# Kernel optimization log

Hardware: AMD Instinct MI355X
Metric: run time of the kernel (lower is better)

## Reference

```python
import jax, jax.numpy as jnp
import numpy as np

B, V, D = 4096, 20, 768


def _conv1d_k3(x, w, b):
    # x: [B, V, D]; single-channel conv1d, kernel=3, padding=1 (torch cross-correlation)
    xp = jnp.pad(x, ((0, 0), (0, 0), (1, 1)))
    return w[0] * xp[..., :-2] + w[1] * xp[..., 1:-1] + w[2] * xp[..., 2:] + b[0]


def setup_inputs() -> dict:
    key = jax.random.key(0)
    ks = jax.random.split(key, 10)
    s = 0.02  # small init scale for weights
    return {
        "text_features": jax.random.normal(ks[0], (B, D), jnp.float32),
        "viewport_features": jax.random.normal(ks[1], (B, V, D), jnp.float32),
        "W1": jax.random.normal(ks[2], (D, D), jnp.float32) * s,
        "b1": jax.random.normal(ks[3], (D,), jnp.float32) * s,
        "W2": jax.random.normal(ks[4], (D, D), jnp.float32) * s,
        "b2": jax.random.normal(ks[5], (D,), jnp.float32) * s,
        "cw1": jax.random.normal(ks[6], (3,), jnp.float32) * 0.5,
        "cb1": jax.random.normal(ks[7], (1,), jnp.float32) * 0.1,
        "cw2": jax.random.normal(ks[8], (3,), jnp.float32) * 0.5,
        "cb2": jax.random.normal(ks[9], (1,), jnp.float32) * 0.1,
    }


def reference(text_features, viewport_features, W1, b1, W2, b2, cw1, cb1, cw2, cb2):
    # Batched over all 20 viewports at once (original loops over i).
    fli_norm = jax.nn.softmax(viewport_features, axis=-1)          # [B,V,D]
    # torch Linear: x @ W.T + b
    m1 = jnp.einsum('bvd,ed->bve', fli_norm, W1) + b1              # mlp1(fli_norm)
    m2 = jnp.einsum('bvd,ed->bve', fli_norm, W2) + b2              # mlp2(fli_norm)
    fused = jax.nn.relu(text_features[:, None, :] * m1 + m2)       # [B,V,D]
    fused = _conv1d_k3(fused, cw1, cb1)
    fused = jax.nn.relu(fused)
    fused = _conv1d_k3(fused, cw2, cb2)
    return fused.reshape(B, V * D)                                 # torch.cat along dim=1
```

## Files before the change

### kernel.cpp

```cpp
#include <hip/hip_runtime.h>

typedef unsigned short u16;
typedef __attribute__((ext_vector_type(8))) short short8;
typedef __attribute__((ext_vector_type(4))) float f32x4;

#define Bn 4096
#define Vn 20
#define Dn 768
#define Mn (Bn * Vn)
#define Nn (2 * Dn)

#define BM 256
#define BNt 256
#define NTILES (Nn / BNt)
#define GRID ((Mn / BM) * NTILES)

typedef __attribute__((address_space(1))) void GV;
typedef __attribute__((address_space(3))) void LV;

__device__ __forceinline__ u16 f2bf(float f) {
  union { float f; unsigned u; } v; v.f = f;
  unsigned r = v.u + 0x7FFFu + ((v.u >> 16) & 1u);
  return (u16)(r >> 16);
}
__device__ __forceinline__ float bf2f(u16 x) {
  union { unsigned u; float f; } v; v.u = ((unsigned)x) << 16; return v.f;
}

__device__ __forceinline__ int lds_off(int r, int hi) {
  return (r >> 1) * 64 + (r & 1) * 32 + ((hi ^ ((r >> 1) & 3)) * 8);
}

__global__ __launch_bounds__(192) void softmax_k(const float* __restrict__ vf,
                                                 u16* __restrict__ X) {
  size_t row = blockIdx.x;
  const float4* p = (const float4*)(vf + row * Dn);
  int t = threadIdx.x;
  float4 v = p[t];
  float mx = fmaxf(fmaxf(v.x, v.y), fmaxf(v.z, v.w));
  #pragma unroll
  for (int off = 32; off; off >>= 1) mx = fmaxf(mx, __shfl_xor(mx, off));
  __shared__ float rr[3];
  __shared__ float rs[3];
  int wv = t >> 6, ln = t & 63;
  if (!ln) rr[wv] = mx;
  __syncthreads();
  mx = fmaxf(fmaxf(rr[0], rr[1]), rr[2]);
  float e0 = __expf(v.x - mx), e1 = __expf(v.y - mx);
  float e2 = __expf(v.z - mx), e3 = __expf(v.w - mx);
  float s = e0 + e1 + e2 + e3;
  #pragma unroll
  for (int off = 32; off; off >>= 1) s += __shfl_xor(s, off);
  if (!ln) rs[wv] = s;
  __syncthreads();
  float inv = 1.0f / (rs[0] + rs[1] + rs[2]);
  ushort4 o;
  o.x = f2bf(e0 * inv); o.y = f2bf(e1 * inv);
  o.z = f2bf(e2 * inv); o.w = f2bf(e3 * inv);
  ((ushort4*)(X + row * Dn))[t] = o;
}

__global__ __launch_bounds__(256) void build_wt_k(const float* __restrict__ W1,
                                                  const float* __restrict__ W2,
                                                  u16* __restrict__ Wt) {
  int idx = blockIdx.x * 256 + threadIdx.x;
  if (idx >= Dn * Dn) return;
  int j = idx / Dn, d = idx - j * Dn;
  int b = j >> 5, c = j & 31;
  Wt[(size_t)(b * 64 + c) * Dn + d]      = f2bf(W1[(size_t)j * Dn + d]);
  Wt[(size_t)(b * 64 + 32 + c) * Dn + d] = f2bf(W2[(size_t)j * Dn + d]);
}

__global__ __launch_bounds__(512, 2) void gemm_fuse_k(
    const u16* __restrict__ X, const u16* __restrict__ Wt,
    const float* __restrict__ b1, const float* __restrict__ b2,
    const float* __restrict__ text, float* __restrict__ out,
    u16* __restrict__ seam,
    const float* __restrict__ cw1, const float* __restrict__ cb1,
    const float* __restrict__ cw2, const float* __restrict__ cb2) {
  __shared__ __align__(16) u16 smem[65536];

  const int h = blockIdx.x;
  const int lin = (h & 7) * (GRID / 8) + (h >> 3);
  const int by = lin / NTILES, bx = lin - by * NTILES;
  const int brow = by * BM;

  const int t = threadIdx.x, w = t >> 6, l = t & 63;
  const int lo = l & 15, hi = l >> 4;
  const int wrr = w >> 2, wcc = w & 3;

  int offA[8], offB[4];
  #pragma unroll
  for (int m = 0; m < 8; ++m) offA[m] = lds_off(wrr * 128 + m * 16 + lo, hi);
  #pragma unroll
  for (int n = 0; n < 4; ++n) offB[n] = lds_off(wcc * 64 + n * 16 + lo, hi);

  const u16* gA[2];
  const u16* gB[2];
  #pragma unroll
  for (int ii = 0; ii < 2; ++ii) {
    int q = ii * 512 + t;
    int rp = q >> 3, half = (q >> 2) & 1, kc = (q & 3) ^ (rp & 3);
    gA[ii] = X + (size_t)(brow + rp * 2 + half) * Dn + kc * 8;
    gB[ii] = Wt + (size_t)(bx * BNt + rp * 2 + half) * Dn + kc * 8;
  }

#define STG_A(DST, KOFF) do { _Pragma("unroll")                                \
    for (int ii = 0; ii < 2; ++ii)                                             \
      __builtin_amdgcn_global_load_lds((GV*)(gA[ii] + (KOFF)),                 \
          (LV*)(smem + (DST) + (ii * 512 + w * 64) * 8), 16, 0, 0); } while (0)
#define STG_B(DST, KOFF) do { _Pragma("unroll")                                \
    for (int ii = 0; ii < 2; ++ii)                                             \
      __builtin_amdgcn_global_load_lds((GV*)(gB[ii] + (KOFF)),                 \
          (LV*)(smem + (DST) + (ii * 512 + w * 64) * 8), 16, 0, 0); } while (0)

  STG_A(0, 0);              STG_B(16384, 0);
  STG_A(32768, 64);         STG_B(49152, 64);
  STG_A(8192, 32);          STG_B(24576, 32);
  STG_A(40960, 96);         STG_B(57344, 96);
  asm volatile("s_waitcnt vmcnt(12)" ::: "memory");
  __builtin_amdgcn_s_barrier();

  f32x4 acc[8][4] = {};
  short8 af[8], bb0, bb1;

#define PH(SB, KH, NH, NEWA, STG, VM) do {                                     \
    if (NEWA) { _Pragma("unroll") for (int m = 0; m < 8; ++m)                  \
      af[m] = *(const short8*)(smem + (SB) + (KH) * 8192 + offA[m]); }         \
    bb0 = *(const short8*)(smem + (SB) + 16384 + (KH) * 8192 + offB[(NH)*2]);  \
    bb1 = *(const short8*)(smem + (SB) + 16384 + (KH) * 8192 + offB[(NH)*2+1]);\
    STG;                                                                       \
    __builtin_amdgcn_s_barrier();                                              \
    asm volatile("s_waitcnt lgkmcnt(0)" ::: "memory");                         \
    __builtin_amdgcn_sched_barrier(0);                                         \
    __builtin_amdgcn_s_setprio(1);                                             \
    _Pragma("unroll") for (int m = 0; m < 8; ++m) {                            \
      acc[m][(NH)*2]   = __builtin_amdgcn_mfma_f32_16x16x32_bf16(af[m], bb0, acc[m][(NH)*2],   0, 0, 0); \
      acc[m][(NH)*2+1] = __builtin_amdgcn_mfma_f32_16x16x32_bf16(af[m], bb1, acc[m][(NH)*2+1], 0, 0, 0); \
    }                                                                          \
    __builtin_amdgcn_s_setprio(0);                                             \
    VM;                                                                        \
    __builtin_amdgcn_s_barrier();                                              \
  } while (0)

#define VM4 asm volatile("s_waitcnt vmcnt(4)" ::: "memory")
#define VM0 asm volatile("s_waitcnt vmcnt(0)" ::: "memory")

  #pragma unroll
  for (int i = 0; i < 6; ++i) {
    const int ka = (2 * i + 1) * 64;
    const int kb = (2 * i + 2) * 64;
    PH(0, 0, 0, true,  if (i >= 1) STG_A(32768, ka),      ;  );
    PH(0, 0, 1, false, if (i >= 1) STG_B(49152, ka),      VM4);
    PH(0, 1, 0, true,  if (i >= 1) STG_A(40960, ka + 32), ;  );
    PH(0, 1, 1, false, if (i >= 1) STG_B(57344, ka + 32), VM4);
    PH(32768, 0, 0, true,  if (i <= 4) STG_A(0, kb),          ;  );
    PH(32768, 0, 1, false, if (i <= 4) STG_B(16384, kb),      if (i == 5) { VM0; } else { VM4; });
    PH(32768, 1, 0, true,  if (i <= 4) STG_A(8192, kb + 32),  ;  );
    PH(32768, 1, 1, false, if (i <= 4) STG_B(24576, kb + 32), if (i <= 4) { VM4; });
  }
#undef PH
#undef VM4
#undef VM0
#undef STG_A
#undef STG_B

  const float w10 = cw1[0], w11 = cw1[1], w12 = cw1[2], c1b = cb1[0];
  const float w20 = cw2[0], w21 = cw2[1], w22 = cw2[2], c2b = cb2[0];

  u16* fsm = smem;
  u16* tsm = smem + 32768;

  #pragma unroll
  for (int n = 0; n < 2; ++n) {
    const int cl = wcc * 32 + n * 16 + lo;
    const int e  = bx * 128 + cl;
    const float B1 = b1[e], B2 = b2[e];
    #pragma unroll
    for (int m = 0; m < 8; ++m) {
      const int rl = wrr * 128 + m * 16 + hi * 4;
      uint2 pk;
      u16* pku = (u16*)&pk;
      #pragma unroll
      for (int r = 0; r < 4; ++r) {
        const int gr = brow + rl + r;
        const float v1 = acc[m][n][r] + B1;
        const float v2 = acc[m][n + 2][r] + B2;
        const float tf = text[(size_t)(gr / Vn) * Dn + e];
        pku[r] = f2bf(fmaxf(tf * v1 + v2, 0.0f));
      }
      *(uint2*)(fsm + cl * 256 + (rl ^ ((cl & 31) << 3))) = pk;
      const int sidx = (cl < 4) ? cl : ((cl >= 124) ? cl - 120 : -1);
      if (sidx >= 0)
        *(uint2*)(seam + ((size_t)(by * 6 + bx) * 8 + sidx) * 256 + rl) = pk;
    }
  }
  __syncthreads();

  const int cl = t & 127, rb = t >> 7;
  const int cL = cl ? cl - 1 : 0, cR = (cl < 127) ? cl + 1 : 127;
  short8 tC[8];
  #pragma unroll
  for (int j = 0; j < 8; ++j) {
    const int R = rb * 64 + j * 8;
    short8 sL = *(const short8*)(fsm + cL * 256 + (R ^ ((cL & 31) << 3)));
    short8 sC = *(const short8*)(fsm + cl * 256 + (R ^ ((cl & 31) << 3)));
    short8 sR = *(const short8*)(fsm + cR * 256 + (R ^ ((cR & 31) << 3)));
    short8 o;
    #pragma unroll
    for (int k = 0; k < 8; ++k) {
      float a = bf2f((u16)sL[k]), b = bf2f((u16)sC[k]), c = bf2f((u16)sR[k]);
      float v = fmaxf(fmaf(w10, a, fmaf(w11, b, fmaf(w12, c, c1b))), 0.0f);
      o[k] = (short)f2bf(v);
    }
    *(short8*)(tsm + cl * 256 + (R ^ ((cl & 31) << 3))) = o;
    tC[j] = o;
  }
  __syncthreads();

  const bool wr_ok = (cl >= 2 && cl <= 125);
  #pragma unroll
  for (int j = 0; j < 8; ++j) {
    const int R = rb * 64 + j * 8;
    short8 tL = *(const short8*)(tsm + cL * 256 + (R ^ ((cL & 31) << 3)));
    short8 tR = *(const short8*)(tsm + cR * 256 + (R ^ ((cR & 31) << 3)));
    #pragma unroll
    for (int k = 0; k < 8; ++k) {
      float v = fmaf(w20, bf2f((u16)tL[k]),
                fmaf(w21, bf2f((u16)tC[j][k]),
                fmaf(w22, bf2f((u16)tR[k]), c2b)));
      if (wr_ok)
        out[(size_t)(brow + R + k) * Dn + bx * 128 + cl] = v;
    }
  }
}

__global__ __launch_bounds__(256) void seam_k(const u16* __restrict__ seam,
                                              float* __restrict__ out,
                                              const float* __restrict__ cw1,
                                              const float* __restrict__ cb1,
                                              const float* __restrict__ cw2,
                                              const float* __restrict__ cb2) {
  const int bid = blockIdx.x;
  const int by = bid / 6, bx = bid - by * 6;
  const int r = threadIdx.x;
  const float w10 = cw1[0], w11 = cw1[1], w12 = cw1[2], c1b = cb1[0];
  const float w20 = cw2[0], w21 = cw2[1], w22 = cw2[2], c2b = cb2[0];
  #define SM(B, I) bf2f(seam[((size_t)(B) * 8 + (I)) * 256 + r])
  float fm2 = 0.f, fm1 = 0.f, fR0 = 0.f, fR1 = 0.f;
  if (bx > 0) { fm2 = SM(bid - 1, 6); fm1 = SM(bid - 1, 7); }
  if (bx < 5) { fR0 = SM(bid + 1, 0); fR1 = SM(bid + 1, 1); }
  const float f0 = SM(bid, 0), f1 = SM(bid, 1), f2 = SM(bid, 2), f3 = SM(bid, 3);
  const float f124 = SM(bid, 4), f125 = SM(bid, 5), f126 = SM(bid, 6), f127 = SM(bid, 7);
  #undef SM
  #define C1(a, b, c) fmaxf(fmaf(w10, (a), fmaf(w11, (b), fmaf(w12, (c), c1b))), 0.0f)
  const float tm1  = (bx > 0) ? C1(fm2, fm1, f0) : 0.0f;
  const float t0   = C1(fm1, f0, f1);
  const float t1   = C1(f0, f1, f2);
  const float t2   = C1(f1, f2, f3);
  const float t125 = C1(f124, f125, f126);
  const float t126 = C1(f125, f126, f127);
  const float t127 = C1(f126, f127, fR0);
  const float t128 = (bx < 5) ? C1(f127, fR0, fR1) : 0.0f;
  #undef C1
  const size_t go = (size_t)(by * 256 + r) * Dn + bx * 128;
  out[go + 0]   = fmaf(w20, tm1,  fmaf(w21, t0,   fmaf(w22, t1,   c2b)));
  out[go + 1]   = fmaf(w20, t0,   fmaf(w21, t1,   fmaf(w22, t2,   c2b)));
  out[go + 126] = fmaf(w20, t125, fmaf(w21, t126, fmaf(w22, t127, c2b)));
  out[go + 127] = fmaf(w20, t126, fmaf(w21, t127, fmaf(w22, t128, c2b)));
}

extern "C" void kernel_launch(void* const* d_in, const int* in_sizes, int n_in,
                              void* d_out, int out_size, void* d_ws, size_t ws_size,
                              hipStream_t stream) {
  const float* text = (const float*)d_in[0];
  const float* vf   = (const float*)d_in[1];
  const float* W1   = (const float*)d_in[2];
  const float* b1   = (const float*)d_in[3];
  const float* W2   = (const float*)d_in[4];
  const float* b2   = (const float*)d_in[5];
  const float* cw1  = (const float*)d_in[6];
  const float* cb1  = (const float*)d_in[7];
  const float* cw2  = (const float*)d_in[8];
  const float* cb2  = (const float*)d_in[9];
  float* out = (float*)d_out;

  u16* X    = (u16*)d_ws;
  u16* Wt   = X + (size_t)Mn * Dn;
  u16* seam = Wt + (size_t)Nn * Dn;

  softmax_k<<<Mn, 192, 0, stream>>>(vf, X);
  build_wt_k<<<(Dn * Dn + 255) / 256, 256, 0, stream>>>(W1, W2, Wt);
  gemm_fuse_k<<<GRID, 512, 0, stream>>>(X, Wt, b1, b2, text, out, seam,
                                        cw1, cb1, cw2, cb2);
  seam_k<<<GRID, 256, 0, stream>>>(seam, out, cw1, cb1, cw2, cb2);
}
```

Measured before the change: 373.8 us.

## Shrink GEMM tile to 256x128 with simpler double-buffered K loop for occupancy

Halves the N tile of the fused GEMM (128 interleaved W1/W2 columns, 64 output features) and cuts LDS to 64KB so four blocks per CU can fit. The hand-scheduled 8-phase K pipeline is replaced by a simple two-slot double buffer over K chunks of 32. The conv epilogue, seam handling and seam kernel are rescaled to 64-column output tiles. In exchange each A tile is reloaded twice as often, more seam columns need fixup, and there is less MFMA work per barrier.

```diff
diff --git a/kernel.cpp b/kernel.cpp
--- a/kernel.cpp
+++ b/kernel.cpp
@@ -11,9 +11,12 @@
 #define Nn (2 * Dn)
 
 #define BM 256
-#define BNt 256
+#define BNt 128
+#define HK 32
+#define NHK (Dn / HK)
 #define NTILES (Nn / BNt)
 #define GRID ((Mn / BM) * NTILES)
+#define SLOTU 12288
 
 typedef __attribute__((address_space(1))) void GV;
 typedef __attribute__((address_space(3))) void LV;
@@ -29,6 +32,9 @@
 
 __device__ __forceinline__ int lds_off(int r, int hi) {
   return (r >> 1) * 64 + (r & 1) * 32 + ((hi ^ ((r >> 1) & 3)) * 8);
+}
+__device__ __forceinline__ int fsw(int c, int r) {
+  return c * 256 + (r ^ ((c & 31) << 3));
 }
 
 __global__ __launch_bounds__(192) void softmax_k(const float* __restrict__ vf,
@@ -71,14 +77,14 @@
   Wt[(size_t)(b * 64 + 32 + c) * Dn + d] = f2bf(W2[(size_t)j * Dn + d]);
 }
 
-__global__ __launch_bounds__(512, 2) void gemm_fuse_k(
+__global__ __launch_bounds__(512, 4) void gemm_fuse_k(
     const u16* __restrict__ X, const u16* __restrict__ Wt,
     const float* __restrict__ b1, const float* __restrict__ b2,
     const float* __restrict__ text, float* __restrict__ out,
     u16* __restrict__ seam,
     const float* __restrict__ cw1, const float* __restrict__ cb1,
     const float* __restrict__ cw2, const float* __restrict__ cb2) {
-  __shared__ __align__(16) u16 smem[65536];
+  __shared__ __align__(16) u16 smem[32768];
 
   const int h = blockIdx.x;
   const int lin = (h & 7) * (GRID / 8) + (h >> 3);
@@ -87,98 +93,80 @@
 
   const int t = threadIdx.x, w = t >> 6, l = t & 63;
   const int lo = l & 15, hi = l >> 4;
-  const int wrr = w >> 2, wcc = w & 3;
-
-  int offA[8], offB[4];
-  #pragma unroll
-  for (int m = 0; m < 8; ++m) offA[m] = lds_off(wrr * 128 + m * 16 + lo, hi);
-  #pragma unroll
-  for (int n = 0; n < 4; ++n) offB[n] = lds_off(wcc * 64 + n * 16 + lo, hi);
+  const int wrr = w >> 1, wcc = w & 1;
+
+  int offA[4], offB[4];
+  #pragma unroll
+  for (int m = 0; m < 4; ++m) offA[m] = lds_off(wrr * 64 + m * 16 + lo, hi);
+  #pragma unroll
+  for (int n = 0; n < 4; ++n) offB[n] = 8192 + lds_off(wcc * 64 + n * 16 + lo, hi);
 
   const u16* gA[2];
-  const u16* gB[2];
+  const u16* gB;
   #pragma unroll
   for (int ii = 0; ii < 2; ++ii) {
     int q = ii * 512 + t;
     int rp = q >> 3, half = (q >> 2) & 1, kc = (q & 3) ^ (rp & 3);
     gA[ii] = X + (size_t)(brow + rp * 2 + half) * Dn + kc * 8;
-    gB[ii] = Wt + (size_t)(bx * BNt + rp * 2 + half) * Dn + kc * 8;
-  }
-
-#define STG_A(DST, KOFF) do { _Pragma("unroll")                                \
+  }
+  {
+    int rp = t >> 3, half = (t >> 2) & 1, kc = (t & 3) ^ (rp & 3);
+    gB = Wt + (size_t)(bx * BNt + rp * 2 + half) * Dn + kc * 8;
+  }
+
+#define STAGE(SLOT, KOFF) do {                                                 \
+    _Pragma("unroll")                                                          \
     for (int ii = 0; ii < 2; ++ii)                                             \
       __builtin_amdgcn_global_load_lds((GV*)(gA[ii] + (KOFF)),                 \
-          (LV*)(smem + (DST) + (ii * 512 + w * 64) * 8), 16, 0, 0); } while (0)
-#define STG_B(DST, KOFF) do { _Pragma("unroll")                                \
-    for (int ii = 0; ii < 2; ++ii)                                             \
-      __builtin_amdgcn_global_load_lds((GV*)(gB[ii] + (KOFF)),                 \
-          (LV*)(smem + (DST) + (ii * 512 + w * 64) * 8), 16, 0, 0); } while (0)
-
-  STG_A(0, 0);              STG_B(16384, 0);
-  STG_A(32768, 64);         STG_B(49152, 64);
-  STG_A(8192, 32);          STG_B(24576, 32);
-  STG_A(40960, 96);         STG_B(57344, 96);
-  asm volatile("s_waitcnt vmcnt(12)" ::: "memory");
-  __builtin_amdgcn_s_barrier();
-
-  f32x4 acc[8][4] = {};
-  short8 af[8], bb0, bb1;
-
-#define PH(SB, KH, NH, NEWA, STG, VM) do {                                     \
-    if (NEWA) { _Pragma("unroll") for (int m = 0; m < 8; ++m)                  \
-      af[m] = *(const short8*)(smem + (SB) + (KH) * 8192 + offA[m]); }         \
-    bb0 = *(const short8*)(smem + (SB) + 16384 + (KH) * 8192 + offB[(NH)*2]);  \
-    bb1 = *(const short8*)(smem + (SB) + 16384 + (KH) * 8192 + offB[(NH)*2+1]);\
-    STG;                                                                       \
-    __builtin_amdgcn_s_barrier();                                              \
-    asm volatile("s_waitcnt lgkmcnt(0)" ::: "memory");                         \
-    __builtin_amdgcn_sched_barrier(0);                                         \
-    __builtin_amdgcn_s_setprio(1);                                             \
-    _Pragma("unroll") for (int m = 0; m < 8; ++m) {                            \
-      acc[m][(NH)*2]   = __builtin_amdgcn_mfma_f32_16x16x32_bf16(af[m], bb0, acc[m][(NH)*2],   0, 0, 0); \
-      acc[m][(NH)*2+1] = __builtin_amdgcn_mfma_f32_16x16x32_bf16(af[m], bb1, acc[m][(NH)*2+1], 0, 0, 0); \
-    }                                                                          \
-    __builtin_amdgcn_s_setprio(0);                                             \
-    VM;                                                                        \
-    __builtin_amdgcn_s_barrier();                                              \
+          (LV*)(smem + (SLOT) * SLOTU + (ii * 512 + t) * 8), 16, 0, 0);        \
+    __builtin_amdgcn_global_load_lds((GV*)(gB + (KOFF)),                       \
+        (LV*)(smem + (SLOT) * SLOTU + 8192 + t * 8), 16, 0, 0);                \
   } while (0)
 
-#define VM4 asm volatile("s_waitcnt vmcnt(4)" ::: "memory")
-#define VM0 asm volatile("s_waitcnt vmcnt(0)" ::: "memory")
-
-  #pragma unroll
-  for (int i = 0; i < 6; ++i) {
-    const int ka = (2 * i + 1) * 64;
-    const int kb = (2 * i + 2) * 64;
-    PH(0, 0, 0, true,  if (i >= 1) STG_A(32768, ka),      ;  );
-    PH(0, 0, 1, false, if (i >= 1) STG_B(49152, ka),      VM4);
-    PH(0, 1, 0, true,  if (i >= 1) STG_A(40960, ka + 32), ;  );
-    PH(0, 1, 1, false, if (i >= 1) STG_B(57344, ka + 32), VM4);
-    PH(32768, 0, 0, true,  if (i <= 4) STG_A(0, kb),          ;  );
-    PH(32768, 0, 1, false, if (i <= 4) STG_B(16384, kb),      if (i == 5) { VM0; } else { VM4; });
-    PH(32768, 1, 0, true,  if (i <= 4) STG_A(8192, kb + 32),  ;  );
-    PH(32768, 1, 1, false, if (i <= 4) STG_B(24576, kb + 32), if (i <= 4) { VM4; });
-  }
-#undef PH
-#undef VM4
-#undef VM0
-#undef STG_A
-#undef STG_B
+  STAGE(0, 0);
+  STAGE(1, HK);
+
+  f32x4 acc[4][4] = {};
+  short8 af[4], bfr[4];
+
+  #pragma unroll 2
+  for (int hk = 0; hk < NHK; ++hk) {
+    if (hk < NHK - 2) asm volatile("s_waitcnt vmcnt(3)" ::: "memory");
+    else              asm volatile("s_waitcnt vmcnt(0)" ::: "memory");
+    __builtin_amdgcn_s_barrier();
+    const u16* sa = smem + (hk & 1) * SLOTU;
+    #pragma unroll
+    for (int m = 0; m < 4; ++m) af[m]  = *(const short8*)(sa + offA[m]);
+    #pragma unroll
+    for (int n = 0; n < 4; ++n) bfr[n] = *(const short8*)(sa + offB[n]);
+    asm volatile("s_waitcnt lgkmcnt(0)" ::: "memory");
+    __builtin_amdgcn_sched_barrier(0);
+    __builtin_amdgcn_s_setprio(1);
+    #pragma unroll
+    for (int m = 0; m < 4; ++m)
+      #pragma unroll
+      for (int n = 0; n < 4; ++n)
+        acc[m][n] = __builtin_amdgcn_mfma_f32_16x16x32_bf16(af[m], bfr[n], acc[m][n], 0, 0, 0);
+    __builtin_amdgcn_s_setprio(0);
+    __builtin_amdgcn_s_barrier();
+    if (hk < NHK - 2) STAGE(hk & 1, (hk + 2) * HK);
+  }
+#undef STAGE
 
   const float w10 = cw1[0], w11 = cw1[1], w12 = cw1[2], c1b = cb1[0];
   const float w20 = cw2[0], w21 = cw2[1], w22 = cw2[2], c2b = cb2[0];
 
   u16* fsm = smem;
-  u16* tsm = smem + 32768;
+  u16* tsm = smem + 16384;
 
   #pragma unroll
   for (int n = 0; n < 2; ++n) {
     const int cl = wcc * 32 + n * 16 + lo;
-    const int e  = bx * 128 + cl;
+    const int e  = bx * 64 + cl;
     const float B1 = b1[e], B2 = b2[e];
     #pragma unroll
-    for (int m = 0; m < 8; ++m) {
-      const int rl = wrr * 128 + m * 16 + hi * 4;
+    for (int m = 0; m < 4; ++m) {
+      const int rl = wrr * 64 + m * 16 + hi * 4;
       uint2 pk;
       u16* pku = (u16*)&pk;
       #pragma unroll
@@ -189,48 +177,47 @@
         const float tf = text[(size_t)(gr / Vn) * Dn + e];
         pku[r] = f2bf(fmaxf(tf * v1 + v2, 0.0f));
       }
-      *(uint2*)(fsm + cl * 256 + (rl ^ ((cl & 31) << 3))) = pk;
-      const int sidx = (cl < 4) ? cl : ((cl >= 124) ? cl - 120 : -1);
+      *(uint2*)(fsm + fsw(cl, rl)) = pk;
+      const int sidx = (cl < 4) ? cl : ((cl >= 60) ? cl - 56 : -1);
       if (sidx >= 0)
-        *(uint2*)(seam + ((size_t)(by * 6 + bx) * 8 + sidx) * 256 + rl) = pk;
+        *(uint2*)(seam + ((size_t)(by * NTILES + bx) * 8 + sidx) * 256 + rl) = pk;
     }
   }
   __syncthreads();
 
-  const int cl = t & 127, rb = t >> 7;
-  const int cL = cl ? cl - 1 : 0, cR = (cl < 127) ? cl + 1 : 127;
-  short8 tC[8];
-  #pragma unroll
-  for (int j = 0; j < 8; ++j) {
-    const int R = rb * 64 + j * 8;
-    short8 sL = *(const short8*)(fsm + cL * 256 + (R ^ ((cL & 31) << 3)));
-    short8 sC = *(const short8*)(fsm + cl * 256 + (R ^ ((cl & 31) << 3)));
-    short8 sR = *(const short8*)(fsm + cR * 256 + (R ^ ((cR & 31) << 3)));
+  const int cl = t & 63, rb = t >> 6;
+  const int cL = cl ? cl - 1 : 0, cR = (cl < 63) ? cl + 1 : 63;
+  short8 tC[4];
+  #pragma unroll
+  for (int j = 0; j < 4; ++j) {
+    const int R = rb * 32 + j * 8;
+    short8 sL = *(const short8*)(fsm + fsw(cL, R));
+    short8 sC = *(const short8*)(fsm + fsw(cl, R));
+    short8 sR = *(const short8*)(fsm + fsw(cR, R));
     short8 o;
     #pragma unroll
     for (int k = 0; k < 8; ++k) {
       float a = bf2f((u16)sL[k]), b = bf2f((u16)sC[k]), c = bf2f((u16)sR[k]);
-      float v = fmaxf(fmaf(w10, a, fmaf(w11, b, fmaf(w12, c, c1b))), 0.0f);
-      o[k] = (short)f2bf(v);
+      o[k] = (short)f2bf(fmaxf(fmaf(w10, a, fmaf(w11, b, fmaf(w12, c, c1b))), 0.0f));
     }
-    *(short8*)(tsm + cl * 256 + (R ^ ((cl & 31) << 3))) = o;
+    *(short8*)(tsm + fsw(cl, R)) = o;
     tC[j] = o;
   }
   __syncthreads();
 
-  const bool wr_ok = (cl >= 2 && cl <= 125);
-  #pragma unroll
-  for (int j = 0; j < 8; ++j) {
-    const int R = rb * 64 + j * 8;
-    short8 tL = *(const short8*)(tsm + cL * 256 + (R ^ ((cL & 31) << 3)));
-    short8 tR = *(const short8*)(tsm + cR * 256 + (R ^ ((cR & 31) << 3)));
+  const bool wr_ok = (cl >= 2 && cl <= 61);
+  #pragma unroll
+  for (int j = 0; j < 4; ++j) {
+    const int R = rb * 32 + j * 8;
+    short8 tL = *(const short8*)(tsm + fsw(cL, R));
+    short8 tR = *(const short8*)(tsm + fsw(cR, R));
     #pragma unroll
     for (int k = 0; k < 8; ++k) {
       float v = fmaf(w20, bf2f((u16)tL[k]),
                 fmaf(w21, bf2f((u16)tC[j][k]),
                 fmaf(w22, bf2f((u16)tR[k]), c2b)));
       if (wr_ok)
-        out[(size_t)(brow + R + k) * Dn + bx * 128 + cl] = v;
+        out[(size_t)(brow + R + k) * Dn + bx * 64 + cl] = v;
     }
   }
 }
@@ -242,32 +229,32 @@
                                               const float* __restrict__ cw2,
                                               const float* __restrict__ cb2) {
   const int bid = blockIdx.x;
-  const int by = bid / 6, bx = bid - by * 6;
+  const int by = bid / NTILES, bx = bid - by * NTILES;
   const int r = threadIdx.x;
   const float w10 = cw1[0], w11 = cw1[1], w12 = cw1[2], c1b = cb1[0];
   const float w20 = cw2[0], w21 = cw2[1], w22 = cw2[2], c2b = cb2[0];
   #define SM(B, I) bf2f(seam[((size_t)(B) * 8 + (I)) * 256 + r])
   float fm2 = 0.f, fm1 = 0.f, fR0 = 0.f, fR1 = 0.f;
-  if (bx > 0) { fm2 = SM(bid - 1, 6); fm1 = SM(bid - 1, 7); }
-  if (bx < 5) { fR0 = SM(bid + 1, 0); fR1 = SM(bid + 1, 1); }
+  if (bx > 0)          { fm2 = SM(bid - 1, 6); fm1 = SM(bid - 1, 7); }
+  if (bx < NTILES - 1) { fR0 = SM(bid + 1, 0); fR1 = SM(bid + 1, 1); }
   const float f0 = SM(bid, 0), f1 = SM(bid, 1), f2 = SM(bid, 2), f3 = SM(bid, 3);
-  const float f124 = SM(bid, 4), f125 = SM(bid, 5), f126 = SM(bid, 6), f127 = SM(bid, 7);
+  const float f60 = SM(bid, 4), f61 = SM(bid, 5), f62 = SM(bid, 6), f63 = SM(bid, 7);
   #undef SM
   #define C1(a, b, c) fmaxf(fmaf(w10, (a), fmaf(w11, (b), fmaf(w12, (c), c1b))), 0.0f)
-  const float tm1  = (bx > 0) ? C1(fm2, fm1, f0) : 0.0f;
-  const float t0   = C1(fm1, f0, f1);
-  const float t1   = C1(f0, f1, f2);
-  const float t2   = C1(f1, f2, f3);
-  const float t125 = C1(f124, f125, f126);
-  const float t126 = C1(f125, f126, f127);
-  const float t127 = C1(f126, f127, fR0);
-  const float t128 = (bx < 5) ? C1(f127, fR0, fR1) : 0.0f;
+  const float tm1 = (bx > 0) ? C1(fm2, fm1, f0) : 0.0f;
+  const float t0  = C1(fm1, f0, f1);
+  const float t1  = C1(f0, f1, f2);
+  const float t2  = C1(f1, f2, f3);
+  const float t61 = C1(f60, f61, f62);
+  const float t62 = C1(f61, f62, f63);
+  const float t63 = C1(f62, f63, fR0);
+  const float t64 = (bx < NTILES - 1) ? C1(f63, fR0, fR1) : 0.0f;
   #undef C1
-  const size_t go = (size_t)(by * 256 + r) * Dn + bx * 128;
-  out[go + 0]   = fmaf(w20, tm1,  fmaf(w21, t0,   fmaf(w22, t1,   c2b)));
-  out[go + 1]   = fmaf(w20, t0,   fmaf(w21, t1,   fmaf(w22, t2,   c2b)));
-  out[go + 126] = fmaf(w20, t125, fmaf(w21, t126, fmaf(w22, t127, c2b)));
-  out[go + 127] = fmaf(w20, t126, fmaf(w21, t127, fmaf(w22, t128, c2b)));
+  const size_t go = (size_t)(by * 256 + r) * Dn + bx * 64;
+  out[go + 0]  = fmaf(w20, tm1, fmaf(w21, t0,  fmaf(w22, t1,  c2b)));
+  out[go + 1]  = fmaf(w20, t0,  fmaf(w21, t1,  fmaf(w22, t2,  c2b)));
+  out[go + 62] = fmaf(w20, t61, fmaf(w21, t62, fmaf(w22, t63, c2b)));
+  out[go + 63] = fmaf(w20, t62, fmaf(w21, t63, fmaf(w22, t64, c2b)));
 }
 
 extern "C" void kernel_launch(void* const* d_in, const int* in_sizes, int n_in,
```

After: 398.5 us. 6.6% more time.

## Switch GEMM operands from bf16 to scaled fp8 with fp8 MFMA

Applied to the files above, without the earlier changes.

The softmax output and the transposed weights are now quantized to fp8 with a fixed scale of 32, and the fused GEMM uses the fp8 MFMA instruction, undoing the scale in the epilogue. This halves intermediate write and read traffic and LDS footprint per k-step, and fp8 MFMA has higher throughput. The LDS swizzle, staging loads and wait counts are reworked for byte-sized elements. Quantizing softmax probabilities (values near 1/768 times 32) and small weights to fp8 risks accuracy loss against the float reference.

```diff
diff --git a/kernel.cpp b/kernel.cpp
--- a/kernel.cpp
+++ b/kernel.cpp
@@ -1,6 +1,7 @@
 #include <hip/hip_runtime.h>
 
 typedef unsigned short u16;
+typedef unsigned char u8;
 typedef __attribute__((ext_vector_type(8))) short short8;
 typedef __attribute__((ext_vector_type(4))) float f32x4;
 
@@ -15,6 +16,9 @@
 #define NTILES (Nn / BNt)
 #define GRID ((Mn / BM) * NTILES)
 
+#define SCL 32.0f
+#define ISCL2 (1.0f / 1024.0f)
+
 typedef __attribute__((address_space(1))) void GV;
 typedef __attribute__((address_space(3))) void LV;
 
@@ -27,12 +31,13 @@
   union { unsigned u; float f; } v; v.u = ((unsigned)x) << 16; return v.f;
 }
 
-__device__ __forceinline__ int lds_off(int r, int hi) {
-  return (r >> 1) * 64 + (r & 1) * 32 + ((hi ^ ((r >> 1) & 3)) * 8);
+__device__ __forceinline__ int lds8(int r, int hi) {
+  return (r >> 2) * 128 + (r & 3) * 32 + ((((hi >> 1) ^ ((r >> 2) & 1))) << 4)
+         + (hi & 1) * 8;
 }
 
 __global__ __launch_bounds__(192) void softmax_k(const float* __restrict__ vf,
-                                                 u16* __restrict__ X) {
+                                                 u8* __restrict__ X8) {
   size_t row = blockIdx.x;
   const float4* p = (const float4*)(vf + row * Dn);
   int t = threadIdx.x;
@@ -53,32 +58,40 @@
   for (int off = 32; off; off >>= 1) s += __shfl_xor(s, off);
   if (!ln) rs[wv] = s;
   __syncthreads();
-  float inv = 1.0f / (rs[0] + rs[1] + rs[2]);
-  ushort4 o;
-  o.x = f2bf(e0 * inv); o.y = f2bf(e1 * inv);
-  o.z = f2bf(e2 * inv); o.w = f2bf(e3 * inv);
-  ((ushort4*)(X + row * Dn))[t] = o;
+  float inv = SCL / (rs[0] + rs[1] + rs[2]);
+  unsigned pk = 0;
+  pk = __builtin_amdgcn_cvt_pk_fp8_f32(e0 * inv, e1 * inv, pk, false);
+  pk = __builtin_amdgcn_cvt_pk_fp8_f32(e2 * inv, e3 * inv, pk, true);
+  ((unsigned*)(X8 + row * Dn))[t] = pk;
 }
 
 __global__ __launch_bounds__(256) void build_wt_k(const float* __restrict__ W1,
                                                   const float* __restrict__ W2,
-                                                  u16* __restrict__ Wt) {
+                                                  u8* __restrict__ Wt8) {
   int idx = blockIdx.x * 256 + threadIdx.x;
-  if (idx >= Dn * Dn) return;
-  int j = idx / Dn, d = idx - j * Dn;
+  if (idx >= Dn * (Dn / 4)) return;
+  int j = idx / (Dn / 4), d4 = (idx - j * (Dn / 4)) * 4;
   int b = j >> 5, c = j & 31;
-  Wt[(size_t)(b * 64 + c) * Dn + d]      = f2bf(W1[(size_t)j * Dn + d]);
-  Wt[(size_t)(b * 64 + 32 + c) * Dn + d] = f2bf(W2[(size_t)j * Dn + d]);
+  float4 a = *(const float4*)(W1 + (size_t)j * Dn + d4);
+  float4 e = *(const float4*)(W2 + (size_t)j * Dn + d4);
+  unsigned p1 = 0, p2 = 0;
+  p1 = __builtin_amdgcn_cvt_pk_fp8_f32(a.x * SCL, a.y * SCL, p1, false);
+  p1 = __builtin_amdgcn_cvt_pk_fp8_f32(a.z * SCL, a.w * SCL, p1, true);
+  p2 = __builtin_amdgcn_cvt_pk_fp8_f32(e.x * SCL, e.y * SCL, p2, false);
+  p2 = __builtin_amdgcn_cvt_pk_fp8_f32(e.z * SCL, e.w * SCL, p2, true);
+  *(unsigned*)(Wt8 + (size_t)(b * 64 + c) * Dn + d4)      = p1;
+  *(unsigned*)(Wt8 + (size_t)(b * 64 + 32 + c) * Dn + d4) = p2;
 }
 
 __global__ __launch_bounds__(512, 2) void gemm_fuse_k(
-    const u16* __restrict__ X, const u16* __restrict__ Wt,
+    const u8* __restrict__ X8, const u8* __restrict__ Wt8,
     const float* __restrict__ b1, const float* __restrict__ b2,
     const float* __restrict__ text, float* __restrict__ out,
     u16* __restrict__ seam,
     const float* __restrict__ cw1, const float* __restrict__ cb1,
     const float* __restrict__ cw2, const float* __restrict__ cb2) {
   __shared__ __align__(16) u16 smem[65536];
+  u8* smem8 = (u8*)smem;
 
   const int h = blockIdx.x;
   const int lin = (h & 7) * (GRID / 8) + (h >> 3);
@@ -91,59 +104,54 @@
 
   int offA[8], offB[4];
   #pragma unroll
-  for (int m = 0; m < 8; ++m) offA[m] = lds_off(wrr * 128 + m * 16 + lo, hi);
-  #pragma unroll
-  for (int n = 0; n < 4; ++n) offB[n] = lds_off(wcc * 64 + n * 16 + lo, hi);
-
-  const u16* gA[2];
-  const u16* gB[2];
-  #pragma unroll
-  for (int ii = 0; ii < 2; ++ii) {
-    int q = ii * 512 + t;
-    int rp = q >> 3, half = (q >> 2) & 1, kc = (q & 3) ^ (rp & 3);
-    gA[ii] = X + (size_t)(brow + rp * 2 + half) * Dn + kc * 8;
-    gB[ii] = Wt + (size_t)(bx * BNt + rp * 2 + half) * Dn + kc * 8;
-  }
-
-#define STG_A(DST, KOFF) do { _Pragma("unroll")                                \
-    for (int ii = 0; ii < 2; ++ii)                                             \
-      __builtin_amdgcn_global_load_lds((GV*)(gA[ii] + (KOFF)),                 \
-          (LV*)(smem + (DST) + (ii * 512 + w * 64) * 8), 16, 0, 0); } while (0)
-#define STG_B(DST, KOFF) do { _Pragma("unroll")                                \
-    for (int ii = 0; ii < 2; ++ii)                                             \
-      __builtin_amdgcn_global_load_lds((GV*)(gB[ii] + (KOFF)),                 \
-          (LV*)(smem + (DST) + (ii * 512 + w * 64) * 8), 16, 0, 0); } while (0)
+  for (int m = 0; m < 8; ++m) offA[m] = lds8(wrr * 128 + m * 16 + lo, hi);
+  #pragma unroll
+  for (int n = 0; n < 4; ++n) offB[n] = lds8(wcc * 64 + n * 16 + lo, hi);
+
+  const u8* gA;
+  const u8* gB;
+  {
+    int r = (t >> 3) * 4 + ((t & 7) >> 1);
+    int c16 = (t & 1) ^ ((t >> 3) & 1);
+    gA = X8 + (size_t)(brow + r) * Dn + c16 * 16;
+    gB = Wt8 + (size_t)(bx * BNt + r) * Dn + c16 * 16;
+  }
+
+#define STG_A(DST, KOFF) __builtin_amdgcn_global_load_lds( \
+    (GV*)(gA + (KOFF)), (LV*)(smem8 + (DST) + w * 1024), 16, 0, 0)
+#define STG_B(DST, KOFF) __builtin_amdgcn_global_load_lds( \
+    (GV*)(gB + (KOFF)), (LV*)(smem8 + (DST) + w * 1024), 16, 0, 0)
 
   STG_A(0, 0);              STG_B(16384, 0);
   STG_A(32768, 64);         STG_B(49152, 64);
   STG_A(8192, 32);          STG_B(24576, 32);
   STG_A(40960, 96);         STG_B(57344, 96);
-  asm volatile("s_waitcnt vmcnt(12)" ::: "memory");
+  asm volatile("s_waitcnt vmcnt(6)" ::: "memory");
   __builtin_amdgcn_s_barrier();
 
   f32x4 acc[8][4] = {};
-  short8 af[8], bb0, bb1;
+  long af[8], bb0, bb1;
 
 #define PH(SB, KH, NH, NEWA, STG, VM) do {                                     \
     if (NEWA) { _Pragma("unroll") for (int m = 0; m < 8; ++m)                  \
-      af[m] = *(const short8*)(smem + (SB) + (KH) * 8192 + offA[m]); }         \
-    bb0 = *(const short8*)(smem + (SB) + 16384 + (KH) * 8192 + offB[(NH)*2]);  \
-    bb1 = *(const short8*)(smem + (SB) + 16384 + (KH) * 8192 + offB[(NH)*2+1]);\
+      af[m] = *(const long*)(smem8 + (SB) + (KH) * 8192 + offA[m]); }          \
+    bb0 = *(const long*)(smem8 + (SB) + 16384 + (KH) * 8192 + offB[(NH)*2]);   \
+    bb1 = *(const long*)(smem8 + (SB) + 16384 + (KH) * 8192 + offB[(NH)*2+1]); \
     STG;                                                                       \
     __builtin_amdgcn_s_barrier();                                              \
     asm volatile("s_waitcnt lgkmcnt(0)" ::: "memory");                         \
     __builtin_amdgcn_sched_barrier(0);                                         \
     __builtin_amdgcn_s_setprio(1);                                             \
     _Pragma("unroll") for (int m = 0; m < 8; ++m) {                            \
-      acc[m][(NH)*2]   = __builtin_amdgcn_mfma_f32_16x16x32_bf16(af[m], bb0, acc[m][(NH)*2],   0, 0, 0); \
-      acc[m][(NH)*2+1] = __builtin_amdgcn_mfma_f32_16x16x32_bf16(af[m], bb1, acc[m][(NH)*2+1], 0, 0, 0); \
+      acc[m][(NH)*2]   = __builtin_amdgcn_mfma_f32_16x16x32_fp8_fp8(af[m], bb0, acc[m][(NH)*2],   0, 0, 0); \
+      acc[m][(NH)*2+1] = __builtin_amdgcn_mfma_f32_16x16x32_fp8_fp8(af[m], bb1, acc[m][(NH)*2+1], 0, 0, 0); \
     }                                                                          \
     __builtin_amdgcn_s_setprio(0);                                             \
     VM;                                                                        \
     __builtin_amdgcn_s_barrier();                                              \
   } while (0)
 
-#define VM4 asm volatile("s_waitcnt vmcnt(4)" ::: "memory")
+#define VM2 asm volatile("s_waitcnt vmcnt(2)" ::: "memory")
 #define VM0 asm volatile("s_waitcnt vmcnt(0)" ::: "memory")
 
   #pragma unroll
@@ -151,16 +159,16 @@
     const int ka = (2 * i + 1) * 64;
     const int kb = (2 * i + 2) * 64;
     PH(0, 0, 0, true,  if (i >= 1) STG_A(32768, ka),      ;  );
-    PH(0, 0, 1, false, if (i >= 1) STG_B(49152, ka),      VM4);
+    PH(0, 0, 1, false, if (i >= 1) STG_B(49152, ka),      VM2);
     PH(0, 1, 0, true,  if (i >= 1) STG_A(40960, ka + 32), ;  );
-    PH(0, 1, 1, false, if (i >= 1) STG_B(57344, ka + 32), VM4);
+    PH(0, 1, 1, false, if (i >= 1) STG_B(57344, ka + 32), VM2);
     PH(32768, 0, 0, true,  if (i <= 4) STG_A(0, kb),          ;  );
-    PH(32768, 0, 1, false, if (i <= 4) STG_B(16384, kb),      if (i == 5) { VM0; } else { VM4; });
+    PH(32768, 0, 1, false, if (i <= 4) STG_B(16384, kb),      if (i == 5) { VM0; } else { VM2; });
     PH(32768, 1, 0, true,  if (i <= 4) STG_A(8192, kb + 32),  ;  );
-    PH(32768, 1, 1, false, if (i <= 4) STG_B(24576, kb + 32), if (i <= 4) { VM4; });
+    PH(32768, 1, 1, false, if (i <= 4) STG_B(24576, kb + 32), if (i <= 4) { VM2; });
   }
 #undef PH
-#undef VM4
+#undef VM2
 #undef VM0
 #undef STG_A
 #undef STG_B
@@ -184,8 +192,8 @@
       #pragma unroll
       for (int r = 0; r < 4; ++r) {
         const int gr = brow + rl + r;
-        const float v1 = acc[m][n][r] + B1;
-        const float v2 = acc[m][n + 2][r] + B2;
+        const float v1 = acc[m][n][r] * ISCL2 + B1;
+        const float v2 = acc[m][n + 2][r] * ISCL2 + B2;
         const float tf = text[(size_t)(gr / Vn) * Dn + e];
         pku[r] = f2bf(fmaxf(tf * v1 + v2, 0.0f));
       }
@@ -285,13 +293,13 @@
   const float* cb2  = (const float*)d_in[9];
   float* out = (float*)d_out;
 
-  u16* X    = (u16*)d_ws;
-  u16* Wt   = X + (size_t)Mn * Dn;
-  u16* seam = Wt + (size_t)Nn * Dn;
-
-  softmax_k<<<Mn, 192, 0, stream>>>(vf, X);
-  build_wt_k<<<(Dn * Dn + 255) / 256, 256, 0, stream>>>(W1, W2, Wt);
-  gemm_fuse_k<<<GRID, 512, 0, stream>>>(X, Wt, b1, b2, text, out, seam,
+  u8*  X8   = (u8*)d_ws;
+  u8*  Wt8  = X8 + (size_t)Mn * Dn;
+  u16* seam = (u16*)(Wt8 + (size_t)Nn * Dn);
+
+  softmax_k<<<Mn, 192, 0, stream>>>(vf, X8);
+  build_wt_k<<<(Dn * (Dn / 4) + 255) / 256, 256, 0, stream>>>(W1, W2, Wt8);
+  gemm_fuse_k<<<GRID, 512, 0, stream>>>(X8, Wt8, b1, b2, text, out, seam,
                                         cw1, cb1, cw2, cb2);
   seam_k<<<GRID, 256, 0, stream>>>(seam, out, cw1, cb1, cw2, cb2);
 }
```

Measured after the change: 346.6 us. -7.3%, faster.
